# Kernel optimization log

Hardware: AMD Instinct MI355X
Metric: run time of the kernel (lower is better)

Reference implementation:

```python
import jax, jax.numpy as jnp
import numpy as np

N = 50000      # nodes
E = 800000     # edges (avg degree 16)
DIN = 128      # input_dim
H = 256        # hidden_channels
DOUT = 64      # output_dim


def _glorot(k, shape):
    lim = float(np.sqrt(6.0 / (shape[0] + shape[1])))
    return jax.random.uniform(k, shape, jnp.float32, -lim, lim)


def setup_inputs() -> dict:
    key = jax.random.key(0)
    ks = jax.random.split(key, 10)
    return {
        "x": jax.random.normal(ks[0], (N, DIN), jnp.float32),
        "W1": _glorot(ks[3], (DIN, H)), "b1": jnp.zeros((H,), jnp.float32),
        "W2": _glorot(ks[4], (H, H)),   "b2": jnp.zeros((H,), jnp.float32),
        "L1w": _glorot(ks[5], (H, DIN)), "L1b": jnp.zeros((DIN,), jnp.float32),
        "L2w": _glorot(ks[6], (DIN, H)), "L2b": jnp.zeros((H,), jnp.float32),
        "W3": _glorot(ks[7], (H, DOUT)), "b3": jnp.zeros((DOUT,), jnp.float32),
        "adj": jax.random.randint(ks[1], (2, E), 0, N),
        "adj2": jax.random.randint(ks[2], (2, E), 0, N),
        "mode": 1,  # 1 -> 'l' (return logits); 0 -> softmax over classes
    }


def gcn_conv(x, edge_index, W, b):
    """PyG-style GCNConv: add self-loops, symmetric D^-1/2 A D^-1/2 norm,
    aggregate neighbor features, then (here fused) linear transform."""
    n = x.shape[0]
    loop = jnp.arange(n)
    src = jnp.concatenate([edge_index[0], loop])  # message sources (j)
    dst = jnp.concatenate([edge_index[1], loop])  # aggregation targets (i)
    deg = jax.ops.segment_sum(jnp.ones(src.shape[0], x.dtype), dst, num_segments=n)
    dinv = jax.lax.rsqrt(jnp.maximum(deg, 1.0))   # deg >= 1 due to self-loops
    norm = dinv[src] * dinv[dst]                  # [E+N]
    h = x @ W                                     # transform first (smaller of the two dims either way)
    msg = h[src] * norm[:, None]                  # gather + scale, [E+N, out]
    return jax.ops.segment_sum(msg, dst, num_segments=n) + b


def reference(x, W1, b1, W2, b2, L1w, L1b, L2w, L2b, W3, b3, adj, adj2, mode):
    h = jax.nn.relu(gcn_conv(x, adj, W1, b1))      # GCNConv(in->h) on adj
    h = jax.nn.relu(gcn_conv(h, adj2, W2, b2))     # GCNConv(h->h) on adj2
    h = jax.nn.relu(h @ L1w + L1b)                 # Linear(h->in)
    h = jax.nn.relu(h @ L2w + L2b)                 # Linear(in->h)
    out = gcn_conv(h, adj2, W3, b3)                # GCNConv(h->out) on adj2
    # dropout has p=0 -> identity
    return out if mode == 1 else jax.nn.softmax(out, axis=1)
```

## Files before the change

### kernel.cpp

```cpp
#include <hip/hip_runtime.h>
#include <hip/hip_bf16.h>
#include <cstdint>
#include <cstddef>

#define NNODES 50000
#define NEDGES 800000
#define D_IN   128
#define D_H    256
#define D_OUT  64
#define BSH    9
#define BKN    (1 << BSH)
#define NBKT   ((NNODES + BKN - 1) / BKN)
#define MAXB   12288
#define CHUNK  2048

typedef __attribute__((ext_vector_type(8))) short bf16x8;
typedef __attribute__((ext_vector_type(4))) float f32x4;

__device__ __forceinline__ unsigned short f2bf(float f) {
    unsigned u = __builtin_bit_cast(unsigned, f);
    unsigned r = (u + 0x7FFFu + ((u >> 16) & 1u)) >> 16;
    return (unsigned short)r;
}
__device__ __forceinline__ float bf2f(unsigned short h) {
    unsigned u = ((unsigned)h) << 16;
    return __builtin_bit_cast(float, u);
}


__global__ __launch_bounds__(256) void k_bin(const int* __restrict__ adjA, const int* __restrict__ adjB,
                                             int* __restrict__ bcnt, unsigned* __restrict__ binned, int e) {
    __shared__ int h[NBKT], pfx[NBKT], put[NBKT], gbase[NBKT];
    __shared__ unsigned stage[CHUNK];
    const int g = blockIdx.y;
    const int* srcp = g ? adjB : adjA;
    const int* dstp = srcp + e;
    unsigned* outp = binned + (size_t)g * NBKT * MAXB;
    int* bc = bcnt + g * NBKT;
    const int tid = threadIdx.x;
    const int base = blockIdx.x * CHUNK;
    const int nrem = min(CHUNK, e - base);
    if (nrem <= 0) return;

    for (int t = tid; t < NBKT; t += 256) { h[t] = 0; put[t] = 0; }
    __syncthreads();

    unsigned pv[8];
    int bv[8];
    #pragma unroll
    for (int q = 0; q < 8; ++q) {
        int i = base + q * 256 + tid;
        bv[q] = -1;
        if (i < e) {
            int s = srcp[i];
            int d = dstp[i];
            pv[q] = ((unsigned)d << 16) | (unsigned)s;
            bv[q] = d >> BSH;
            atomicAdd(&h[bv[q]], 1);
        }
    }
    __syncthreads();
    if (tid == 0) {
        int r = 0;
        for (int k = 0; k < NBKT; ++k) { pfx[k] = r; r += h[k]; }
    }
    __syncthreads();
    #pragma unroll
    for (int q = 0; q < 8; ++q) {
        if (bv[q] >= 0) {
            int p = pfx[bv[q]] + atomicAdd(&put[bv[q]], 1);
            stage[p] = pv[q];
        }
    }
    __syncthreads();
    if (tid < NBKT && h[tid] > 0) gbase[tid] = atomicAdd(&bc[tid], h[tid]);
    __syncthreads();
    for (int idx = tid; idx < nrem; idx += 256) {
        unsigned v = stage[idx];
        int bb = v >> (16 + BSH);
        outp[(size_t)bb * MAXB + gbase[bb] + (idx - pfx[bb])] = v;
    }
}

__global__ void k_bktscan(const int* __restrict__ bcnt, int* __restrict__ bbase,
                          int* __restrict__ rp1, int* __restrict__ rp2) {
    __shared__ int s[2][NBKT];
    int t = threadIdx.x;
    if (t < NBKT) s[0][t] = bcnt[t];
    else if (t < 2 * NBKT) s[1][t - NBKT] = bcnt[t];
    __syncthreads();
    if (t < 2) {
        int r = 0;
        for (int k = 0; k < NBKT; ++k) { int v = s[t][k]; s[t][k] = r; r += v; }
    }
    __syncthreads();
    if (t < NBKT) bbase[t] = s[0][t];
    else if (t < 2 * NBKT) bbase[t] = s[1][t - NBKT];
    if (t == 0) { rp1[NNODES] = NEDGES; rp2[NNODES] = NEDGES; }
}

__global__ __launch_bounds__(256) void k_csr_bucket(const unsigned* __restrict__ binned,
                                                    const int* __restrict__ bcnt, const int* __restrict__ bbase,
                                                    int* __restrict__ rp1, int* __restrict__ rp2,
                                                    float* __restrict__ dinv1, float* __restrict__ dinv2,
                                                    int* __restrict__ col1, int* __restrict__ col2, int n) {
    __shared__ int lc[BKN];
    __shared__ int loff[BKN];
    __shared__ int ps[256];
    __shared__ int srt[MAXB];
    const int g = blockIdx.y;
    const int b = blockIdx.x;
    const unsigned* in = binned + (size_t)g * NBKT * MAXB + (size_t)b * MAXB;
    int* rp = g ? rp2 : rp1;
    float* dinv = g ? dinv2 : dinv1;
    int* col = g ? col2 : col1;
    const int nb = bcnt[g * NBKT + b];
    const int base0 = bbase[g * NBKT + b];
    const int nodebase = b << BSH;
    const int tid = threadIdx.x;

    for (int t = tid; t < BKN; t += 256) lc[t] = 0;
    __syncthreads();
    for (int t = tid; t < nb; t += 256)
        atomicAdd(&lc[(in[t] >> 16) & (BKN - 1)], 1);
    __syncthreads();
    int c0 = lc[2 * tid], c1 = lc[2 * tid + 1];
    int pair = c0 + c1;
    int sum = pair;
    ps[tid] = pair;
    __syncthreads();
    #pragma unroll
    for (int off = 1; off < 256; off <<= 1) {
        int u = (tid >= off) ? ps[tid - off] : 0;
        __syncthreads();
        sum += u;
        ps[tid] = sum;
        __syncthreads();
    }
    int excl = sum - pair;
    loff[2 * tid] = excl;
    loff[2 * tid + 1] = excl + c0;
    __syncthreads();
    for (int t = tid; t < BKN; t += 256) {
        int node = nodebase + t;
        if (node < n) {
            rp[node] = base0 + loff[t];
            dinv[node] = rsqrtf((float)(lc[t] + 1));
        }
    }
    __syncthreads();
    for (int t = tid; t < nb; t += 256) {
        unsigned v = in[t];
        int pos = atomicAdd(&loff[(v >> 16) & (BKN - 1)], 1);
        srt[pos] = (int)(v & 0xFFFFu);
    }
    __syncthreads();
    for (int t = tid; t < nb; t += 256) col[base0 + t] = srt[t];
}


template<int F, bool PRESCALE>
__global__ __launch_bounds__(256) void k_quant(const float* __restrict__ in, const float* __restrict__ dscale,
                                               short* __restrict__ q, float* __restrict__ qs, int n) {
    constexpr int VPT = F / 64;
    const int lane = threadIdx.x & 63;
    const int i = blockIdx.x * 4 + (threadIdx.x >> 6);
    if (i >= n) return;
    float v[VPT];
    const float* p = in + (size_t)i * F + lane * VPT;
    if constexpr (VPT == 4) { float4 t = *(const float4*)p; v[0] = t.x; v[1] = t.y; v[2] = t.z; v[3] = t.w; }
    else if constexpr (VPT == 2) { float2 t = *(const float2*)p; v[0] = t.x; v[1] = t.y; }
    else v[0] = *p;
    if constexpr (PRESCALE) {
        float d = dscale[i];
        #pragma unroll
        for (int c = 0; c < VPT; ++c) v[c] *= d;
    }
    float m = 0.f;
    #pragma unroll
    for (int c = 0; c < VPT; ++c) m = fmaxf(m, fabsf(v[c]));
    #pragma unroll
    for (int off = 32; off > 0; off >>= 1) m = fmaxf(m, __shfl_xor(m, off));
    float inv = (m > 0.f) ? 32767.0f / m : 0.f;
    short* qp = q + (size_t)i * F + lane * VPT;
    if constexpr (VPT == 4) {
        short4 o;
        o.x = (short)__float2int_rn(v[0] * inv);
        o.y = (short)__float2int_rn(v[1] * inv);
        o.z = (short)__float2int_rn(v[2] * inv);
        o.w = (short)__float2int_rn(v[3] * inv);
        *(short4*)qp = o;
    } else if constexpr (VPT == 2) {
        short2 o;
        o.x = (short)__float2int_rn(v[0] * inv);
        o.y = (short)__float2int_rn(v[1] * inv);
        *(short2*)qp = o;
    } else {
        *qp = (short)__float2int_rn(v[0] * inv);
    }
    if (lane == 0) qs[i] = m * (1.0f / 32767.0f);
}


template<int F, int OUTM>
__global__ __launch_bounds__(256) void k_agg3(const short* __restrict__ q, const float* __restrict__ qs,
                                              const int* __restrict__ rp, const int* __restrict__ col,
                                              const float* __restrict__ dinv, const float* __restrict__ bias,
                                              void* __restrict__ outv, int n) {
    constexpr int VPT = F / 64;
    const int lane = threadIdx.x & 63;
    const int i = blockIdx.x * 4 + (threadIdx.x >> 6);
    if (i >= n) return;
    const short* ql = q + lane * VPT;
    float acc[VPT];
    #pragma unroll
    for (int c = 0; c < VPT; ++c) acc[c] = 0.f;

    int k = rp[i], end = rp[i + 1];

    auto body1 = [&](int j) {
        float s = qs[j];
        const short* pj = ql + (size_t)j * F;
        if constexpr (VPT == 4) {
            short4 v = *(const short4*)pj;
            acc[0] += s * (float)v.x; acc[1] += s * (float)v.y;
            acc[2] += s * (float)v.z; acc[3] += s * (float)v.w;
        } else if constexpr (VPT == 2) {
            short2 v = *(const short2*)pj;
            acc[0] += s * (float)v.x; acc[1] += s * (float)v.y;
        } else {
            acc[0] += s * (float)(*pj);
        }
    };

    body1(i);
    for (; k + 4 <= end; k += 4) {
        int j0 = col[k], j1 = col[k + 1], j2 = col[k + 2], j3 = col[k + 3];
        float s0 = qs[j0], s1 = qs[j1], s2 = qs[j2], s3 = qs[j3];
        if constexpr (VPT == 4) {
            short4 v0 = *(const short4*)(ql + (size_t)j0 * F);
            short4 v1 = *(const short4*)(ql + (size_t)j1 * F);
            short4 v2 = *(const short4*)(ql + (size_t)j2 * F);
            short4 v3 = *(const short4*)(ql + (size_t)j3 * F);
            acc[0] += s0 * (float)v0.x + s1 * (float)v1.x + s2 * (float)v2.x + s3 * (float)v3.x;
            acc[1] += s0 * (float)v0.y + s1 * (float)v1.y + s2 * (float)v2.y + s3 * (float)v3.y;
            acc[2] += s0 * (float)v0.z + s1 * (float)v1.z + s2 * (float)v2.z + s3 * (float)v3.z;
            acc[3] += s0 * (float)v0.w + s1 * (float)v1.w + s2 * (float)v2.w + s3 * (float)v3.w;
        } else if constexpr (VPT == 2) {
            short2 v0 = *(const short2*)(ql + (size_t)j0 * F);
            short2 v1 = *(const short2*)(ql + (size_t)j1 * F);
            short2 v2 = *(const short2*)(ql + (size_t)j2 * F);
            short2 v3 = *(const short2*)(ql + (size_t)j3 * F);
            acc[0] += s0 * (float)v0.x + s1 * (float)v1.x + s2 * (float)v2.x + s3 * (float)v3.x;
            acc[1] += s0 * (float)v0.y + s1 * (float)v1.y + s2 * (float)v2.y + s3 * (float)v3.y;
        } else {
            float v0 = (float)ql[(size_t)j0 * F];
            float v1 = (float)ql[(size_t)j1 * F];
            float v2 = (float)ql[(size_t)j2 * F];
            float v3 = (float)ql[(size_t)j3 * F];
            acc[0] += s0 * v0 + s1 * v1 + s2 * v2 + s3 * v3;
        }
    }
    for (; k < end; ++k) body1(col[k]);

    float di = dinv[i];
    if constexpr (OUTM == 0) {
        unsigned short* o = (unsigned short*)outv + (size_t)i * 2 * F + lane * VPT;
        #pragma unroll
        for (int c = 0; c < VPT; ++c) {
            float val = acc[c] * di;
            unsigned short h = f2bf(val);
            unsigned short l = f2bf(val - bf2f(h));
            o[c] = h;
            o[F + c] = l;
        }
    } else {
        float* o = (float*)outv + (size_t)i * F + lane * VPT;
        #pragma unroll
        for (int c = 0; c < VPT; ++c) o[c] = acc[c] * di + bias[lane * VPT + c];
    }
}


__device__ __forceinline__ void wconv1(const float* __restrict__ W, unsigned short* __restrict__ Th,
                                       unsigned short* __restrict__ Tl, int idx, int K, int Nc) {
    int k = idx / Nc, n = idx - k * Nc;
    float v = W[idx];
    unsigned short h = f2bf(v);
    unsigned short l = f2bf(v - bf2f(h));
    Th[(size_t)n * K + k] = h;
    Tl[(size_t)n * K + k] = l;
}

__global__ void k_wconv_all(const float* W1, const float* W2, const float* L1w, const float* L2w, const float* W3,
                            unsigned short* W1h, unsigned short* W1l, unsigned short* W2h, unsigned short* W2l,
                            unsigned short* L1h, unsigned short* L1l, unsigned short* L2h, unsigned short* L2l,
                            unsigned short* W3h, unsigned short* W3l) {
    int idx = blockIdx.x * blockDim.x + threadIdx.x;
    if (idx < 32768)        wconv1(W1, W1h, W1l, idx, D_IN, D_H);
    else if (idx < 98304)   wconv1(W2, W2h, W2l, idx - 32768, D_H, D_H);
    else if (idx < 131072)  wconv1(L1w, L1h, L1l, idx - 98304, D_H, D_IN);
    else if (idx < 163840)  wconv1(L2w, L2h, L2l, idx - 131072, D_IN, D_H);
    else if (idx < 180224)  wconv1(W3, W3h, W3l, idx - 163840, D_H, D_OUT);
}


template<bool RELU, bool BIAS, int OUTM>
__global__ __launch_bounds__(256) void k_gemm3(const unsigned short* __restrict__ Ahl,
        const unsigned short* __restrict__ Bth, const unsigned short* __restrict__ Btl,
        const float* __restrict__ bias, const float* __restrict__ dscale,
        void* __restrict__ Cv, int M, int K, int Nc, int ncb) {
    constexpr int PAD = 66;
    __shared__ unsigned short As_h[128][PAD];
    __shared__ unsigned short As_l[128][PAD];
    __shared__ unsigned short Bs_h[64][PAD];
    __shared__ unsigned short Bs_l[64][PAD];

    const int nwg = gridDim.x;
    const int b = blockIdx.x;
    const int q8 = nwg >> 3, r8 = nwg & 7;
    const int xcd = b & 7;
    const int swz = (xcd < r8 ? xcd * (q8 + 1) : r8 * (q8 + 1) + (xcd - r8) * q8) + (b >> 3);
    const int row0 = (swz / ncb) * 128;
    const int col0 = (swz % ncb) * 64;

    const int tid = threadIdx.x;
    const int lane = tid & 63;
    const int wv = tid >> 6;

    f32x4 acc[2][4];
    #pragma unroll
    for (int m = 0; m < 2; ++m)
        #pragma unroll
        for (int n = 0; n < 4; ++n) acc[m][n] = (f32x4)(0.f);

    const int srow = tid >> 1;
    const int skh = (tid & 1) * 32;
    int arow = row0 + srow;
    if (arow >= M) arow = M - 1;
    const unsigned short* aph = Ahl + (size_t)arow * 2 * K + skh;
    const unsigned short* apl = aph + K;

    const int bn = tid >> 2;
    const int bko = (tid & 3) * 16;
    const unsigned short* bph = Bth + (size_t)(col0 + bn) * K + bko;
    const unsigned short* bpl = Btl + (size_t)(col0 + bn) * K + bko;

    const int fr = lane & 15;
    const int fk = (lane >> 4) * 8;

    const int nk = K >> 6;
    for (int kt = 0; kt < nk; ++kt) {
        uint4 ah0 = *(const uint4*)(aph + kt * 64);
        uint4 ah1 = *(const uint4*)(aph + kt * 64 + 8);
        uint4 ah2 = *(const uint4*)(aph + kt * 64 + 16);
        uint4 ah3 = *(const uint4*)(aph + kt * 64 + 24);
        uint4 al0 = *(const uint4*)(apl + kt * 64);
        uint4 al1 = *(const uint4*)(apl + kt * 64 + 8);
        uint4 al2 = *(const uint4*)(apl + kt * 64 + 16);
        uint4 al3 = *(const uint4*)(apl + kt * 64 + 24);
        uint4 bh0 = *(const uint4*)(bph + kt * 64);
        uint4 bh1 = *(const uint4*)(bph + kt * 64 + 8);
        uint4 bl0 = *(const uint4*)(bpl + kt * 64);
        uint4 bl1 = *(const uint4*)(bpl + kt * 64 + 8);

        __syncthreads();

        *(uint4*)&As_h[srow][skh] = ah0;
        *(uint4*)&As_h[srow][skh + 8] = ah1;
        *(uint4*)&As_h[srow][skh + 16] = ah2;
        *(uint4*)&As_h[srow][skh + 24] = ah3;
        *(uint4*)&As_l[srow][skh] = al0;
        *(uint4*)&As_l[srow][skh + 8] = al1;
        *(uint4*)&As_l[srow][skh + 16] = al2;
        *(uint4*)&As_l[srow][skh + 24] = al3;
        *(uint4*)&Bs_h[bn][bko] = bh0;
        *(uint4*)&Bs_h[bn][bko + 8] = bh1;
        *(uint4*)&Bs_l[bn][bko] = bl0;
        *(uint4*)&Bs_l[bn][bko + 8] = bl1;

        __syncthreads();

        #pragma unroll
        for (int ks = 0; ks < 2; ++ks) {
            const int ko = ks * 32 + fk;
            bf16x8 ah[2], al[2], bh[4], bl[4];
            #pragma unroll
            for (int m = 0; m < 2; ++m) {
                ah[m] = *(const bf16x8*)&As_h[wv * 32 + m * 16 + fr][ko];
                al[m] = *(const bf16x8*)&As_l[wv * 32 + m * 16 + fr][ko];
            }
            #pragma unroll
            for (int n = 0; n < 4; ++n) {
                bh[n] = *(const bf16x8*)&Bs_h[n * 16 + fr][ko];
                bl[n] = *(const bf16x8*)&Bs_l[n * 16 + fr][ko];
            }
            #pragma unroll
            for (int m = 0; m < 2; ++m)
                #pragma unroll
                for (int n = 0; n < 4; ++n) {
                    acc[m][n] = __builtin_amdgcn_mfma_f32_16x16x32_bf16(ah[m], bh[n], acc[m][n], 0, 0, 0);
                    acc[m][n] = __builtin_amdgcn_mfma_f32_16x16x32_bf16(ah[m], bl[n], acc[m][n], 0, 0, 0);
                    acc[m][n] = __builtin_amdgcn_mfma_f32_16x16x32_bf16(al[m], bh[n], acc[m][n], 0, 0, 0);
                }
        }
    }

    float bv[4];
    #pragma unroll
    for (int n = 0; n < 4; ++n) bv[n] = BIAS ? bias[col0 + n * 16 + fr] : 0.f;
    const int rbase = row0 + wv * 32 + (lane >> 4) * 4;
    #pragma unroll
    for (int m = 0; m < 2; ++m) {
        #pragma unroll
        for (int j = 0; j < 4; ++j) {
            const int r = rbase + m * 16 + j;
            if (r >= M) continue;
            float ds = 1.f;
            if constexpr (OUTM == 1) ds = dscale[r];
            #pragma unroll
            for (int n = 0; n < 4; ++n) {
                const int c = col0 + n * 16 + fr;
                float o = acc[m][n][j] + bv[n];
                if constexpr (RELU) o = fmaxf(o, 0.f);
                if constexpr (OUTM == 1) {
                    ((float*)Cv)[(size_t)r * Nc + c] = o * ds;
                } else {
                    unsigned short h = f2bf(o);
                    unsigned short l = f2bf(o - bf2f(h));
                    unsigned short* C2 = (unsigned short*)Cv + (size_t)r * 2 * Nc + c;
                    C2[0] = h;
                    C2[Nc] = l;
                }
            }
        }
    }
}


__global__ __launch_bounds__(256) void k_softmax(float* __restrict__ out, const int* __restrict__ mode, int n) {
    if (*mode == 1) return;
    int lane = threadIdx.x & 63;
    int i = blockIdx.x * 4 + (threadIdx.x >> 6);
    if (i >= n) return;
    float v = out[(size_t)i * 64 + lane];
    float m = v;
    #pragma unroll
    for (int off = 32; off > 0; off >>= 1) m = fmaxf(m, __shfl_xor(m, off));
    float e = __expf(v - m);
    float s = e;
    #pragma unroll
    for (int off = 32; off > 0; off >>= 1) s += __shfl_xor(s, off);
    out[(size_t)i * 64 + lane] = e / s;
}


extern "C" void kernel_launch(void* const* d_in, const int* in_sizes, int n_in,
                              void* d_out, int out_size, void* d_ws, size_t ws_size,
                              hipStream_t stream) {
    const float* x   = (const float*)d_in[0];
    const float* W1  = (const float*)d_in[1];
    const float* b1  = (const float*)d_in[2];
    const float* W2  = (const float*)d_in[3];
    const float* b2  = (const float*)d_in[4];
    const float* L1w = (const float*)d_in[5];
    const float* L1b = (const float*)d_in[6];
    const float* L2w = (const float*)d_in[7];
    const float* L2b = (const float*)d_in[8];
    const float* W3  = (const float*)d_in[9];
    const float* b3  = (const float*)d_in[10];
    const int* adj   = (const int*)d_in[11];
    const int* adj2  = (const int*)d_in[12];
    const int* mode  = (const int*)d_in[13];
    float* out = (float*)d_out;

    char* ws = (char*)d_ws;
    auto alloc = [&](size_t bytes) {
        char* p = ws;
        ws += (bytes + 255) & ~(size_t)255;
        return p;
    };
    char*  bufA  = alloc((size_t)NNODES * 256 * 4);
    char*  bufB  = alloc((size_t)NNODES * 256 * 4);
    int*   rp1   = (int*)alloc((NNODES + 1) * 4);
    int*   col1  = (int*)alloc((size_t)NEDGES * 4);
    int*   rp2   = (int*)alloc((NNODES + 1) * 4);
    int*   col2  = (int*)alloc((size_t)NEDGES * 4);
    float* dinv1 = (float*)alloc(NNODES * 4);
    float* dinv2 = (float*)alloc(NNODES * 4);
    int*   bcnt  = (int*)alloc(2 * NBKT * 4);
    int*   bbase = (int*)alloc(2 * NBKT * 4);
    float* qs    = (float*)alloc(NNODES * 4);
    unsigned short* W1h = (unsigned short*)alloc(D_IN * D_H * 2);
    unsigned short* W1l = (unsigned short*)alloc(D_IN * D_H * 2);
    unsigned short* W2h = (unsigned short*)alloc(D_H * D_H * 2);
    unsigned short* W2l = (unsigned short*)alloc(D_H * D_H * 2);
    unsigned short* L1h = (unsigned short*)alloc(D_H * D_IN * 2);
    unsigned short* L1l = (unsigned short*)alloc(D_H * D_IN * 2);
    unsigned short* L2h = (unsigned short*)alloc(D_IN * D_H * 2);
    unsigned short* L2l = (unsigned short*)alloc(D_IN * D_H * 2);
    unsigned short* W3h = (unsigned short*)alloc(D_H * D_OUT * 2);
    unsigned short* W3l = (unsigned short*)alloc(D_H * D_OUT * 2);
    unsigned* binned = (unsigned*)bufA;

    const int AGB = (NNODES + 3) / 4;
    const int MT = (NNODES + 127) / 128;
    const int BINB = (NEDGES + CHUNK - 1) / CHUNK;

    k_wconv_all<<<(180224 + 255) / 256, 256, 0, stream>>>(W1, W2, L1w, L2w, W3,
        W1h, W1l, W2h, W2l, L1h, L1l, L2h, L2l, W3h, W3l);

    hipMemsetAsync(bcnt, 0, 2 * NBKT * 4, stream);
    k_bin<<<dim3(BINB, 2), 256, 0, stream>>>(adj, adj2, bcnt, binned, NEDGES);
    k_bktscan<<<1, 256, 0, stream>>>(bcnt, bbase, rp1, rp2);
    k_csr_bucket<<<dim3(NBKT, 2), 256, 0, stream>>>(binned, bcnt, bbase, rp1, rp2,
                                                    dinv1, dinv2, col1, col2, NNODES);

    k_quant<128, true><<<AGB, 256, 0, stream>>>(x, dinv1, (short*)bufA, qs, NNODES);
    k_agg3<128, 0><<<AGB, 256, 0, stream>>>((const short*)bufA, qs, rp1, col1, dinv1, nullptr, bufB, NNODES);
    k_gemm3<true, true, 1><<<MT * 4, 256, 0, stream>>>(
        (const unsigned short*)bufB, W1h, W1l, b1, dinv2, bufA, NNODES, D_IN, D_H, 4);
    k_quant<256, false><<<AGB, 256, 0, stream>>>((const float*)bufA, nullptr, (short*)bufB, qs, NNODES);
    k_agg3<256, 0><<<AGB, 256, 0, stream>>>((const short*)bufB, qs, rp2, col2, dinv2, nullptr, bufA, NNODES);
    k_gemm3<true, true, 2><<<MT * 4, 256, 0, stream>>>(
        (const unsigned short*)bufA, W2h, W2l, b2, nullptr, bufB, NNODES, D_H, D_H, 4);
    k_gemm3<true, true, 2><<<MT * 2, 256, 0, stream>>>(
        (const unsigned short*)bufB, L1h, L1l, L1b, nullptr, bufA, NNODES, D_H, D_IN, 2);
    k_gemm3<true, true, 2><<<MT * 4, 256, 0, stream>>>(
        (const unsigned short*)bufA, L2h, L2l, L2b, nullptr, bufB, NNODES, D_IN, D_H, 4);
    k_gemm3<false, false, 1><<<MT * 1, 256, 0, stream>>>(
        (const unsigned short*)bufB, W3h, W3l, nullptr, dinv2, bufA, NNODES, D_H, D_OUT, 1);
    k_quant<64, false><<<AGB, 256, 0, stream>>>((const float*)bufA, nullptr, (short*)bufB, qs, NNODES);
    k_agg3<64, 1><<<AGB, 256, 0, stream>>>((const short*)bufB, qs, rp2, col2, dinv2, b3, out, NNODES);
    k_softmax<<<AGB, 256, 0, stream>>>(out, mode, NNODES);
}
```

Measured before the change: 351.9 us.

## Switch first two GCN GEMMs to split int8 MFMA with per-row/column scales

The aggregation kernel now quantizes its output per row to a 16-bit integer split into high and low int8 planes, replacing the bf16 hi/lo pair. W1 and W2 are quantized per column the same way. A new int8 MFMA GEMM computes the three cross products (hh, mixed, ll) and rescales them. This halves the operand bytes and uses int8 matrix throughput in place of three bf16 MFMAs. In exchange it adds a fourth MFMA per tile and lowers precision to about 16-bit fixed point per row.

```diff
diff --git a/kernel.cpp b/kernel.cpp
--- a/kernel.cpp
+++ b/kernel.cpp
@@ -13,9 +13,11 @@
 #define NBKT   ((NNODES + BKN - 1) / BKN)
 #define MAXB   12288
 #define CHUNK  2048
+#define QMAX   32639.0f
 
 typedef __attribute__((ext_vector_type(8))) short bf16x8;
 typedef __attribute__((ext_vector_type(4))) float f32x4;
+typedef __attribute__((ext_vector_type(4))) int   i32x4;
 
 __device__ __forceinline__ unsigned short f2bf(float f) {
     unsigned u = __builtin_bit_cast(unsigned, f);
@@ -206,7 +208,7 @@
 __global__ __launch_bounds__(256) void k_agg3(const short* __restrict__ q, const float* __restrict__ qs,
                                               const int* __restrict__ rp, const int* __restrict__ col,
                                               const float* __restrict__ dinv, const float* __restrict__ bias,
-                                              void* __restrict__ outv, int n) {
+                                              void* __restrict__ outv, float* __restrict__ qs_out, int n) {
     constexpr int VPT = F / 64;
     const int lane = threadIdx.x & 63;
     const int i = blockIdx.x * 4 + (threadIdx.x >> 6);
@@ -265,15 +267,35 @@
 
     float di = dinv[i];
     if constexpr (OUTM == 0) {
-        unsigned short* o = (unsigned short*)outv + (size_t)i * 2 * F + lane * VPT;
+        float vals[VPT];
+        float m = 0.f;
+        #pragma unroll
+        for (int c = 0; c < VPT; ++c) { vals[c] = acc[c] * di; m = fmaxf(m, fabsf(vals[c])); }
+        #pragma unroll
+        for (int off = 32; off > 0; off >>= 1) m = fmaxf(m, __shfl_xor(m, off));
+        float inv = (m > 0.f) ? QMAX / m : 0.f;
+        unsigned ph = 0, pl = 0;
         #pragma unroll
         for (int c = 0; c < VPT; ++c) {
-            float val = acc[c] * di;
-            unsigned short h = f2bf(val);
-            unsigned short l = f2bf(val - bf2f(h));
-            o[c] = h;
-            o[F + c] = l;
-        }
+            int qv = __float2int_rn(vals[c] * inv);
+            int ah = (qv + 128) >> 8;
+            int al = qv - (ah << 8);
+            ph |= (unsigned)(ah & 0xFF) << (8 * c);
+            pl |= (unsigned)(al & 0xFF) << (8 * c);
+        }
+        unsigned char* o8h = (unsigned char*)outv;
+        unsigned char* o8l = o8h + (size_t)n * F;
+        if constexpr (VPT == 4) {
+            *(unsigned*)(o8h + (size_t)i * F + lane * 4) = ph;
+            *(unsigned*)(o8l + (size_t)i * F + lane * 4) = pl;
+        } else if constexpr (VPT == 2) {
+            *(unsigned short*)(o8h + (size_t)i * F + lane * 2) = (unsigned short)ph;
+            *(unsigned short*)(o8l + (size_t)i * F + lane * 2) = (unsigned short)pl;
+        } else {
+            o8h[(size_t)i * F + lane] = (unsigned char)ph;
+            o8l[(size_t)i * F + lane] = (unsigned char)pl;
+        }
+        if (lane == 0) qs_out[i] = m * (1.0f / QMAX);
     } else {
         float* o = (float*)outv + (size_t)i * F + lane * VPT;
         #pragma unroll
@@ -292,16 +314,169 @@
     Tl[(size_t)n * K + k] = l;
 }
 
-__global__ void k_wconv_all(const float* W1, const float* W2, const float* L1w, const float* L2w, const float* W3,
-                            unsigned short* W1h, unsigned short* W1l, unsigned short* W2h, unsigned short* W2l,
+__global__ void k_wconv_all(const float* L1w, const float* L2w, const float* W3,
                             unsigned short* L1h, unsigned short* L1l, unsigned short* L2h, unsigned short* L2l,
                             unsigned short* W3h, unsigned short* W3l) {
     int idx = blockIdx.x * blockDim.x + threadIdx.x;
-    if (idx < 32768)        wconv1(W1, W1h, W1l, idx, D_IN, D_H);
-    else if (idx < 98304)   wconv1(W2, W2h, W2l, idx - 32768, D_H, D_H);
-    else if (idx < 131072)  wconv1(L1w, L1h, L1l, idx - 98304, D_H, D_IN);
-    else if (idx < 163840)  wconv1(L2w, L2h, L2l, idx - 131072, D_IN, D_H);
-    else if (idx < 180224)  wconv1(W3, W3h, W3l, idx - 163840, D_H, D_OUT);
+    if (idx < 32768)        wconv1(L1w, L1h, L1l, idx, D_H, D_IN);
+    else if (idx < 65536)   wconv1(L2w, L2h, L2l, idx - 32768, D_IN, D_H);
+    else if (idx < 81920)   wconv1(W3, W3h, W3l, idx - 65536, D_H, D_OUT);
+}
+
+
+__global__ __launch_bounds__(256) void k_wconv_i8(const float* __restrict__ W1, const float* __restrict__ W2,
+        signed char* __restrict__ B1h, signed char* __restrict__ B1l,
+        signed char* __restrict__ B2h, signed char* __restrict__ B2l,
+        float* __restrict__ ws1, float* __restrict__ ws2) {
+    const int c4 = blockIdx.x * 4 + (threadIdx.x >> 6);
+    const int lane = threadIdx.x & 63;
+    const float* W; signed char *Bh, *Bl; float* ws; int K, c;
+    if (c4 < 256) { W = W1; Bh = B1h; Bl = B1l; ws = ws1; K = D_IN; c = c4; }
+    else          { W = W2; Bh = B2h; Bl = B2l; ws = ws2; K = D_H;  c = c4 - 256; }
+    float m = 0.f;
+    for (int k = lane; k < K; k += 64) m = fmaxf(m, fabsf(W[(size_t)k * D_H + c]));
+    #pragma unroll
+    for (int off = 32; off > 0; off >>= 1) m = fmaxf(m, __shfl_xor(m, off));
+    float inv = (m > 0.f) ? QMAX / m : 0.f;
+    for (int k = lane; k < K; k += 64) {
+        int qv = __float2int_rn(W[(size_t)k * D_H + c] * inv);
+        int ah = (qv + 128) >> 8;
+        int al = qv - (ah << 8);
+        Bh[(size_t)c * K + k] = (signed char)ah;
+        Bl[(size_t)c * K + k] = (signed char)al;
+    }
+    if (lane == 0) ws[c] = m * (1.0f / QMAX);
+}
+
+
+template<bool RELU, bool BIAS, int OUTM>
+__global__ __launch_bounds__(256) void k_gemm_i8(const unsigned char* __restrict__ A8,
+        const float* __restrict__ qsr,
+        const signed char* __restrict__ B8h, const signed char* __restrict__ B8l,
+        const float* __restrict__ wsc,
+        const float* __restrict__ bias, const float* __restrict__ dscale,
+        void* __restrict__ Cv, int M, int K, int Nc, int ncb) {
+    constexpr int PADB = 68;
+    __shared__ unsigned char As_h[128][PADB];
+    __shared__ unsigned char As_l[128][PADB];
+    __shared__ unsigned char Bs_h[64][PADB];
+    __shared__ unsigned char Bs_l[64][PADB];
+
+    const int nwg = gridDim.x;
+    const int b = blockIdx.x;
+    const int q8 = nwg >> 3, r8 = nwg & 7;
+    const int xcd = b & 7;
+    const int swz = (xcd < r8 ? xcd * (q8 + 1) : r8 * (q8 + 1) + (xcd - r8) * q8) + (b >> 3);
+    const int row0 = (swz / ncb) * 128;
+    const int col0 = (swz % ncb) * 64;
+
+    const int tid = threadIdx.x;
+    const int lane = tid & 63;
+    const int wv = tid >> 6;
+
+    i32x4 acc_hh[2][4], acc_mm[2][4], acc_ll[2][4];
+    #pragma unroll
+    for (int m = 0; m < 2; ++m)
+        #pragma unroll
+        for (int n = 0; n < 4; ++n) {
+            acc_hh[m][n] = (i32x4)(0);
+            acc_mm[m][n] = (i32x4)(0);
+            acc_ll[m][n] = (i32x4)(0);
+        }
+
+    const int srow = tid >> 1;
+    const int skh = (tid & 1) * 32;
+    int arow = row0 + srow;
+    if (arow >= M) arow = M - 1;
+    const unsigned char* aph = A8 + (size_t)arow * K + skh;
+    const unsigned char* apl = aph + (size_t)M * K;
+
+    const int bn = tid >> 2;
+    const int bko = (tid & 3) * 16;
+    const signed char* bph = B8h + (size_t)(col0 + bn) * K + bko;
+    const signed char* bpl = B8l + (size_t)(col0 + bn) * K + bko;
+
+    const int fr = lane & 15;
+    const int fko = (lane >> 4) * 16;
+
+    const int nk = K >> 6;
+    for (int kt = 0; kt < nk; ++kt) {
+        uint4 ah0 = *(const uint4*)(aph + kt * 64);
+        uint4 ah1 = *(const uint4*)(aph + kt * 64 + 16);
+        uint4 al0 = *(const uint4*)(apl + kt * 64);
+        uint4 al1 = *(const uint4*)(apl + kt * 64 + 16);
+        uint4 bh0 = *(const uint4*)(bph + kt * 64);
+        uint4 bl0 = *(const uint4*)(bpl + kt * 64);
+
+        __syncthreads();
+
+        *(uint4*)&As_h[srow][skh] = ah0;
+        *(uint4*)&As_h[srow][skh + 16] = ah1;
+        *(uint4*)&As_l[srow][skh] = al0;
+        *(uint4*)&As_l[srow][skh + 16] = al1;
+        *(uint4*)&Bs_h[bn][bko] = bh0;
+        *(uint4*)&Bs_l[bn][bko] = bl0;
+
+        __syncthreads();
+
+        i32x4 fah[2], fal[2], fbh[4], fbl[4];
+        #pragma unroll
+        for (int m = 0; m < 2; ++m) {
+            fah[m] = *(const i32x4*)&As_h[wv * 32 + m * 16 + fr][fko];
+            fal[m] = *(const i32x4*)&As_l[wv * 32 + m * 16 + fr][fko];
+        }
+        #pragma unroll
+        for (int n = 0; n < 4; ++n) {
+            fbh[n] = *(const i32x4*)&Bs_h[n * 16 + fr][fko];
+            fbl[n] = *(const i32x4*)&Bs_l[n * 16 + fr][fko];
+        }
+        #pragma unroll
+        for (int m = 0; m < 2; ++m)
+            #pragma unroll
+            for (int n = 0; n < 4; ++n) {
+                acc_hh[m][n] = __builtin_amdgcn_mfma_i32_16x16x64_i8(fah[m], fbh[n], acc_hh[m][n], 0, 0, 0);
+                acc_mm[m][n] = __builtin_amdgcn_mfma_i32_16x16x64_i8(fah[m], fbl[n], acc_mm[m][n], 0, 0, 0);
+                acc_mm[m][n] = __builtin_amdgcn_mfma_i32_16x16x64_i8(fal[m], fbh[n], acc_mm[m][n], 0, 0, 0);
+                acc_ll[m][n] = __builtin_amdgcn_mfma_i32_16x16x64_i8(fal[m], fbl[n], acc_ll[m][n], 0, 0, 0);
+            }
+    }
+
+    float bv[4], wv_[4];
+    #pragma unroll
+    for (int n = 0; n < 4; ++n) {
+        const int c = col0 + n * 16 + fr;
+        bv[n] = BIAS ? bias[c] : 0.f;
+        wv_[n] = wsc[c];
+    }
+    const int rbase = row0 + wv * 32 + (lane >> 4) * 4;
+    #pragma unroll
+    for (int m = 0; m < 2; ++m) {
+        #pragma unroll
+        for (int j = 0; j < 4; ++j) {
+            const int r = rbase + m * 16 + j;
+            if (r >= M) continue;
+            const float qr = qsr[r];
+            float ds = 1.f;
+            if constexpr (OUTM == 1) ds = dscale[r];
+            #pragma unroll
+            for (int n = 0; n < 4; ++n) {
+                const int c = col0 + n * 16 + fr;
+                float dot = 65536.f * (float)acc_hh[m][n][j] + 256.f * (float)acc_mm[m][n][j]
+                          + (float)acc_ll[m][n][j];
+                float o = dot * qr * wv_[n] + bv[n];
+                if constexpr (RELU) o = fmaxf(o, 0.f);
+                if constexpr (OUTM == 1) {
+                    ((float*)Cv)[(size_t)r * Nc + c] = o * ds;
+                } else {
+                    unsigned short h = f2bf(o);
+                    unsigned short l = f2bf(o - bf2f(h));
+                    unsigned short* C2 = (unsigned short*)Cv + (size_t)r * 2 * Nc + c;
+                    C2[0] = h;
+                    C2[Nc] = l;
+                }
+            }
+        }
+    }
 }
 
 
@@ -490,11 +665,14 @@
     float* dinv2 = (float*)alloc(NNODES * 4);
     int*   bcnt  = (int*)alloc(2 * NBKT * 4);
     int*   bbase = (int*)alloc(2 * NBKT * 4);
-    float* qs    = (float*)alloc(NNODES * 4);
-    unsigned short* W1h = (unsigned short*)alloc(D_IN * D_H * 2);
-    unsigned short* W1l = (unsigned short*)alloc(D_IN * D_H * 2);
-    unsigned short* W2h = (unsigned short*)alloc(D_H * D_H * 2);
-    unsigned short* W2l = (unsigned short*)alloc(D_H * D_H * 2);
+    float* qsA   = (float*)alloc(NNODES * 4);
+    float* qsB   = (float*)alloc(NNODES * 4);
+    signed char* B1h = (signed char*)alloc(256 * D_IN);
+    signed char* B1l = (signed char*)alloc(256 * D_IN);
+    signed char* B2h = (signed char*)alloc(256 * D_H);
+    signed char* B2l = (signed char*)alloc(256 * D_H);
+    float* ws1 = (float*)alloc(256 * 4);
+    float* ws2 = (float*)alloc(256 * 4);
     unsigned short* L1h = (unsigned short*)alloc(D_H * D_IN * 2);
     unsigned short* L1l = (unsigned short*)alloc(D_H * D_IN * 2);
     unsigned short* L2h = (unsigned short*)alloc(D_IN * D_H * 2);
@@ -507,8 +685,9 @@
     const int MT = (NNODES + 127) / 128;
     const int BINB = (NEDGES + CHUNK - 1) / CHUNK;
 
-    k_wconv_all<<<(180224 + 255) / 256, 256, 0, stream>>>(W1, W2, L1w, L2w, W3,
-        W1h, W1l, W2h, W2l, L1h, L1l, L2h, L2l, W3h, W3l);
+    k_wconv_all<<<(81920 + 255) / 256, 256, 0, stream>>>(L1w, L2w, W3,
+        L1h, L1l, L2h, L2l, W3h, W3l);
+    k_wconv_i8<<<128, 256, 0, stream>>>(W1, W2, B1h, B1l, B2h, B2l, ws1, ws2);
 
     hipMemsetAsync(bcnt, 0, 2 * NBKT * 4, stream);
     k_bin<<<dim3(BINB, 2), 256, 0, stream>>>(adj, adj2, bcnt, binned, NEDGES);
@@ -516,21 +695,21 @@
     k_csr_bucket<<<dim3(NBKT, 2), 256, 0, stream>>>(binned, bcnt, bbase, rp1, rp2,
                                                     dinv1, dinv2, col1, col2, NNODES);
 
-    k_quant<128, true><<<AGB, 256, 0, stream>>>(x, dinv1, (short*)bufA, qs, NNODES);
-    k_agg3<128, 0><<<AGB, 256, 0, stream>>>((const short*)bufA, qs, rp1, col1, dinv1, nullptr, bufB, NNODES);
-    k_gemm3<true, true, 1><<<MT * 4, 256, 0, stream>>>(
-        (const unsigned short*)bufB, W1h, W1l, b1, dinv2, bufA, NNODES, D_IN, D_H, 4);
-    k_quant<256, false><<<AGB, 256, 0, stream>>>((const float*)bufA, nullptr, (short*)bufB, qs, NNODES);
-    k_agg3<256, 0><<<AGB, 256, 0, stream>>>((const short*)bufB, qs, rp2, col2, dinv2, nullptr, bufA, NNODES);
-    k_gemm3<true, true, 2><<<MT * 4, 256, 0, stream>>>(
-        (const unsigned short*)bufA, W2h, W2l, b2, nullptr, bufB, NNODES, D_H, D_H, 4);
+    k_quant<128, true><<<AGB, 256, 0, stream>>>(x, dinv1, (short*)bufA, qsA, NNODES);
+    k_agg3<128, 0><<<AGB, 256, 0, stream>>>((const short*)bufA, qsA, rp1, col1, dinv1, nullptr, bufB, qsB, NNODES);
+    k_gemm_i8<true, true, 1><<<MT * 4, 256, 0, stream>>>(
+        (const unsigned char*)bufB, qsB, B1h, B1l, ws1, b1, dinv2, bufA, NNODES, D_IN, D_H, 4);
+    k_quant<256, false><<<AGB, 256, 0, stream>>>((const float*)bufA, nullptr, (short*)bufB, qsA, NNODES);
+    k_agg3<256, 0><<<AGB, 256, 0, stream>>>((const short*)bufB, qsA, rp2, col2, dinv2, nullptr, bufA, qsB, NNODES);
+    k_gemm_i8<true, true, 2><<<MT * 4, 256, 0, stream>>>(
+        (const unsigned char*)bufA, qsB, B2h, B2l, ws2, b2, nullptr, bufB, NNODES, D_H, D_H, 4);
     k_gemm3<true, true, 2><<<MT * 2, 256, 0, stream>>>(
         (const unsigned short*)bufB, L1h, L1l, L1b, nullptr, bufA, NNODES, D_H, D_IN, 2);
     k_gemm3<true, true, 2><<<MT * 4, 256, 0, stream>>>(
         (const unsigned short*)bufA, L2h, L2l, L2b, nullptr, bufB, NNODES, D_IN, D_H, 4);
     k_gemm3<false, false, 1><<<MT * 1, 256, 0, stream>>>(
         (const unsigned short*)bufB, W3h, W3l, nullptr, dinv2, bufA, NNODES, D_H, D_OUT, 1);
-    k_quant<64, false><<<AGB, 256, 0, stream>>>((const float*)bufA, nullptr, (short*)bufB, qs, NNODES);
-    k_agg3<64, 1><<<AGB, 256, 0, stream>>>((const short*)bufB, qs, rp2, col2, dinv2, b3, out, NNODES);
+    k_quant<64, false><<<AGB, 256, 0, stream>>>((const float*)bufA, nullptr, (short*)bufB, qsA, NNODES);
+    k_agg3<64, 1><<<AGB, 256, 0, stream>>>((const short*)bufB, qsA, rp2, col2, dinv2, b3, out, nullptr, NNODES);
     k_softmax<<<AGB, 256, 0, stream>>>(out, mode, NNODES);
 }
```

New measurement: 353.8 us. No clear change (+0.6%).
